# Performance work log

Hardware: AMD Instinct MI355X
Metric: run time of the kernel (lower is better)

## Reference

```python
import jax, jax.numpy as jnp
import numpy as np

NUM_SKILLS = 50000
HIDDEN = 64
B, T = 8192, 1024
EPS = 1e-6


def setup_inputs() -> dict:
    key = jax.random.key(0)
    ks = jax.random.split(key, 8)
    X = jax.random.randint(ks[0], (B,), 0, NUM_SKILLS)
    y = jax.random.randint(ks[1], (B, T), 0, 2, dtype=jnp.int32)
    embed = jax.random.normal(ks[2], (NUM_SKILLS, HIDDEN), jnp.float32)
    bound = 1.0 / np.sqrt(HIDDEN)
    W0 = jax.random.uniform(ks[3], (HIDDEN, HIDDEN), jnp.float32, -bound, bound)
    b0 = jnp.zeros((HIDDEN,), jnp.float32)
    W1 = jax.random.uniform(ks[4], (HIDDEN, HIDDEN), jnp.float32, -bound, bound)
    b1 = jnp.zeros((HIDDEN,), jnp.float32)
    Wout = jax.random.uniform(ks[5], (HIDDEN, 4), jnp.float32, -bound, bound)
    bout = jnp.zeros((4,), jnp.float32)
    return {"X": X, "y": y, "embed": embed, "W0": W0, "b0": b0,
            "W1": W1, "b1": b1, "Wout": Wout, "bout": bout}


def reference(X, y, embed, W0, b0, W1, b1, Wout, bout):
    # Per-student BKT params from embedding + 2-layer MLP + sigmoid, clamped
    h = embed[X]                                   # (B, H)
    h = jax.nn.relu(h @ W0 + b0)
    h = jax.nn.relu(h @ W1 + b1)
    params = jnp.clip(jax.nn.sigmoid(h @ Wout + bout), EPS, 1.0 - EPS)  # (B, 4)
    l, g, s, prior = params[:, 0], params[:, 1], params[:, 2], params[:, 3]

    def step(latent, y_t):
        true_correct = jnp.where(y_t == -1, 0, y_t)
        correct = latent * (1.0 - s) + (1.0 - latent) * g
        k_t1 = latent * (1.0 - s) / correct
        k_t0 = latent * s / (latent * s + (1.0 - latent) * (1.0 - g))
        k_t = jnp.where(true_correct > 0.5, k_t1, k_t0)
        next_latent = jnp.clip(k_t + (1.0 - k_t) * l, EPS, 1.0 - EPS)
        return next_latent, (correct, latent)

    _, (corrects, latents) = jax.lax.scan(step, prior, y.T)  # scan over T
    return corrects.T, latents.T                            # (B, T) each
```

## Files before the change

kernel.cpp:

```cpp
#include <hip/hip_runtime.h>

#define HIDDEN 64
#define TSTEPS 1024
#define NROWS  8192
#define NCHUNK 16
#define CLEN   64
#define KEPS   1e-6f

__global__ __launch_bounds__(64) void bkt_mlp_kernel(
    const int* __restrict__ X, const float* __restrict__ embed,
    const float* __restrict__ W0, const float* __restrict__ b0,
    const float* __restrict__ W1, const float* __restrict__ b1,
    const float* __restrict__ Wout, const float* __restrict__ bout,
    float4* __restrict__ params)
{
    const int row = blockIdx.x;
    const int j   = threadIdx.x;
    __shared__ float sh[HIDDEN];

    const int skill = X[row];
    sh[j] = embed[skill * HIDDEN + j];
    __syncthreads();

    float acc = b0[j];
    #pragma unroll
    for (int k = 0; k < HIDDEN; ++k)
        acc = fmaf(sh[k], W0[k * HIDDEN + j], acc);
    float h0 = fmaxf(acc, 0.0f);
    __syncthreads();
    sh[j] = h0;
    __syncthreads();

    acc = b1[j];
    #pragma unroll
    for (int k = 0; k < HIDDEN; ++k)
        acc = fmaf(sh[k], W1[k * HIDDEN + j], acc);
    float h1 = fmaxf(acc, 0.0f);

    float p0 = h1 * Wout[j * 4 + 0];
    float p1 = h1 * Wout[j * 4 + 1];
    float p2 = h1 * Wout[j * 4 + 2];
    float p3 = h1 * Wout[j * 4 + 3];
    #pragma unroll
    for (int off = 32; off >= 1; off >>= 1) {
        p0 += __shfl_down(p0, off, 64);
        p1 += __shfl_down(p1, off, 64);
        p2 += __shfl_down(p2, off, 64);
        p3 += __shfl_down(p3, off, 64);
    }
    if (j == 0) {
        float v0 = p0 + bout[0], v1 = p1 + bout[1], v2 = p2 + bout[2], v3 = p3 + bout[3];
        float4 r;
        r.x = fminf(fmaxf(1.0f / (1.0f + __expf(-v0)), KEPS), 1.0f - KEPS);
        r.y = fminf(fmaxf(1.0f / (1.0f + __expf(-v1)), KEPS), 1.0f - KEPS);
        r.z = fminf(fmaxf(1.0f / (1.0f + __expf(-v2)), KEPS), 1.0f - KEPS);
        r.w = fminf(fmaxf(1.0f / (1.0f + __expf(-v3)), KEPS), 1.0f - KEPS);
        params[row] = r;
    }
}

__global__ __launch_bounds__(64) void bkt_chunk_mats(
    const int* __restrict__ y, const float4* __restrict__ params,
    float4* __restrict__ Mbuf, unsigned long long* __restrict__ maskbuf)
{
    const int lane = threadIdx.x;
    const int base = blockIdx.x * 64;
    const int c    = blockIdx.y;
    const int t0   = c * CLEN;

    unsigned long long mask = 0ull;
    #pragma unroll 8
    for (int r = 0; r < 64; ++r) {
        int val = y[(size_t)(base + r) * TSTEPS + t0 + lane];
        unsigned long long bal = __ballot(val > 0);
        if (lane == r) mask = bal;
    }

    const float4 p = params[base + lane];
    const float l = p.x, g = p.y, s = p.z;
    const float c1 = 1.f - s - g, d1 = g;
    const float e00_1 = fmaf(l, c1, (1.f - l) * (1.f - s));
    const float e01_1 = l * d1;
    const float c0 = s + g - 1.f, d0 = 1.f - g;
    const float e00_0 = fmaf(l, c0, (1.f - l) * s);
    const float e01_0 = l * d0;

    float m00 = 1.f, m01 = 0.f, m10 = 0.f, m11 = 1.f;
    #pragma unroll
    for (int tt = 0; tt < CLEN; ++tt) {
        const bool one = (mask >> tt) & 1ull;
        const float e00 = one ? e00_1 : e00_0;
        const float e01 = one ? e01_1 : e01_0;
        const float e10 = one ? c1 : c0;
        const float e11 = one ? d1 : d0;
        float n00 = fmaf(e00, m00, e01 * m10);
        float n01 = fmaf(e00, m01, e01 * m11);
        float n10 = fmaf(e10, m00, e11 * m10);
        float n11 = fmaf(e10, m01, e11 * m11);
        if ((tt & 3) == 3) {
            float inv = __builtin_amdgcn_rcpf(n11);
            m00 = n00 * inv; m01 = n01 * inv; m10 = n10 * inv; m11 = 1.f;
        } else {
            m00 = n00; m01 = n01; m10 = n10; m11 = n11;
        }
    }
    Mbuf  [(size_t)c * NROWS + base + lane] = make_float4(m00, m01, m10, m11);
    maskbuf[(size_t)c * NROWS + base + lane] = mask;
}

__global__ __launch_bounds__(256) void bkt_chunk_starts(
    const float4* __restrict__ params, const float4* __restrict__ Mbuf,
    float* __restrict__ L0buf)
{
    const int r = blockIdx.x * 256 + threadIdx.x;
    float L = params[r].w;
    #pragma unroll
    for (int c = 0; c < NCHUNK; ++c) {
        L0buf[(size_t)c * NROWS + r] = L;
        float4 M = Mbuf[(size_t)c * NROWS + r];
        float num = fmaf(M.x, L, M.y);
        float den = fmaf(M.z, L, M.w);
        L = num * __builtin_amdgcn_rcpf(den);
        L = fminf(fmaxf(L, KEPS), 1.f - KEPS);
    }
}

__global__ __launch_bounds__(64) void bkt_chunk_scan(
    const float4* __restrict__ params, const unsigned long long* __restrict__ maskbuf,
    const float* __restrict__ L0buf,
    float* __restrict__ out_corr, float* __restrict__ out_lat)
{
    const int lane = threadIdx.x;
    const int base = blockIdx.x * 64;
    const int c    = blockIdx.y;
    const int row  = base + lane;

    __shared__ float scor[64][17];
    __shared__ float slat[64][17];

    const float4 p = params[row];
    const float l = p.x, g = p.y, s = p.z;
    const float a   = 1.f - s;
    const float c1v = a - g;
    const float omg = 1.f - g;
    const float c2v = s - omg;
    const float oml = 1.f - l;

    const unsigned long long mask = maskbuf[(size_t)c * NROWS + row];
    float L = L0buf[(size_t)c * NROWS + row];

    const int subr = lane >> 4;
    const int tq   = lane & 15;

    for (int gq = 0; gq < 4; ++gq) {
        #pragma unroll
        for (int q = 0; q < 16; ++q) {
            const int tt = gq * 16 + q;
            const float correct = fmaf(L, c1v, g);
            const float den0    = fmaf(L, c2v, omg);
            const float k1 = (L * a) * __builtin_amdgcn_rcpf(correct);
            const float k0 = (L * s) * __builtin_amdgcn_rcpf(den0);
            const bool one = (mask >> tt) & 1ull;
            const float k = one ? k1 : k0;
            scor[lane][q] = correct;
            slat[lane][q] = L;
            L = fminf(fmaxf(fmaf(k, oml, l), KEPS), 1.f - KEPS);
        }
        __syncthreads();
        #pragma unroll
        for (int it = 0; it < 16; ++it) {
            const int rr = it * 4 + subr;
            const size_t o = (size_t)(base + rr) * TSTEPS + c * CLEN + gq * 16 + tq;
            out_corr[o] = scor[rr][tq];
            out_lat [o] = slat[rr][tq];
        }
        __syncthreads();
    }
}

extern "C" void kernel_launch(void* const* d_in, const int* in_sizes, int n_in,
                              void* d_out, int out_size, void* d_ws, size_t ws_size,
                              hipStream_t stream) {
    const int*   X     = (const int*)  d_in[0];
    const int*   y     = (const int*)  d_in[1];
    const float* embed = (const float*)d_in[2];
    const float* W0    = (const float*)d_in[3];
    const float* b0    = (const float*)d_in[4];
    const float* W1    = (const float*)d_in[5];
    const float* b1    = (const float*)d_in[6];
    const float* Wout  = (const float*)d_in[7];
    const float* bout  = (const float*)d_in[8];

    float* out_corr = (float*)d_out;
    float* out_lat  = out_corr + (size_t)NROWS * TSTEPS;

    char* ws = (char*)d_ws;
    float4*             paramsb = (float4*)(ws);
    float4*             Mbuf    = (float4*)(ws + (128 << 10));
    unsigned long long* maskbuf = (unsigned long long*)(ws + (128 << 10) + (2 << 20));
    float*              L0buf   = (float*)(ws + (128 << 10) + (3 << 20));

    bkt_mlp_kernel<<<NROWS, 64, 0, stream>>>(X, embed, W0, b0, W1, b1, Wout, bout, paramsb);
    bkt_chunk_mats<<<dim3(NROWS / 64, NCHUNK), 64, 0, stream>>>(y, paramsb, Mbuf, maskbuf);
    bkt_chunk_starts<<<NROWS / 256, 256, 0, stream>>>(paramsb, Mbuf, L0buf);
    bkt_chunk_scan<<<dim3(NROWS / 64, NCHUNK), 64, 0, stream>>>(paramsb, maskbuf, L0buf, out_corr, out_lat);
}
```

Baseline: 141.7 us.

## Fuse MLP, chunk matrices, chunk-start scan and output scan into one kernel

```diff
diff --git a/kernel.cpp b/kernel.cpp
--- a/kernel.cpp
+++ b/kernel.cpp
@@ -1,83 +1,113 @@
 #include <hip/hip_runtime.h>
 
-#define HIDDEN 64
 #define TSTEPS 1024
 #define NROWS  8192
 #define NCHUNK 16
 #define CLEN   64
 #define KEPS   1e-6f
 
-__global__ __launch_bounds__(64) void bkt_mlp_kernel(
-    const int* __restrict__ X, const float* __restrict__ embed,
+__global__ __launch_bounds__(64) void bkt_fused(
+    const int* __restrict__ X, const int* __restrict__ y,
+    const float* __restrict__ embed,
     const float* __restrict__ W0, const float* __restrict__ b0,
     const float* __restrict__ W1, const float* __restrict__ b1,
     const float* __restrict__ Wout, const float* __restrict__ bout,
-    float4* __restrict__ params)
+    float* __restrict__ out_corr, float* __restrict__ out_lat)
 {
-    const int row = blockIdx.x;
-    const int j   = threadIdx.x;
-    __shared__ float sh[HIDDEN];
-
-    const int skill = X[row];
-    sh[j] = embed[skill * HIDDEN + j];
+    const int lane    = threadIdx.x;
+    const int rowbase = blockIdx.x * 4;
+
+    __shared__ float sh[4][64];
+
+    #pragma unroll
+    for (int rs = 0; rs < 4; ++rs) {
+        const int skill = X[rowbase + rs];
+        sh[rs][lane] = embed[(size_t)skill * 64 + lane];
+    }
     __syncthreads();
 
-    float acc = b0[j];
-    #pragma unroll
-    for (int k = 0; k < HIDDEN; ++k)
-        acc = fmaf(sh[k], W0[k * HIDDEN + j], acc);
-    float h0 = fmaxf(acc, 0.0f);
+    float a0 = b0[lane], a1 = a0, a2 = a0, a3 = a0;
+    #pragma unroll
+    for (int k4 = 0; k4 < 16; ++k4) {
+        const float4 e0 = *(const float4*)&sh[0][k4 * 4];
+        const float4 e1 = *(const float4*)&sh[1][k4 * 4];
+        const float4 e2 = *(const float4*)&sh[2][k4 * 4];
+        const float4 e3 = *(const float4*)&sh[3][k4 * 4];
+        const float w0 = W0[(k4 * 4 + 0) * 64 + lane];
+        const float w1 = W0[(k4 * 4 + 1) * 64 + lane];
+        const float w2 = W0[(k4 * 4 + 2) * 64 + lane];
+        const float w3 = W0[(k4 * 4 + 3) * 64 + lane];
+        a0 = fmaf(e0.x, w0, a0); a0 = fmaf(e0.y, w1, a0); a0 = fmaf(e0.z, w2, a0); a0 = fmaf(e0.w, w3, a0);
+        a1 = fmaf(e1.x, w0, a1); a1 = fmaf(e1.y, w1, a1); a1 = fmaf(e1.z, w2, a1); a1 = fmaf(e1.w, w3, a1);
+        a2 = fmaf(e2.x, w0, a2); a2 = fmaf(e2.y, w1, a2); a2 = fmaf(e2.z, w2, a2); a2 = fmaf(e2.w, w3, a2);
+        a3 = fmaf(e3.x, w0, a3); a3 = fmaf(e3.y, w1, a3); a3 = fmaf(e3.z, w2, a3); a3 = fmaf(e3.w, w3, a3);
+    }
     __syncthreads();
-    sh[j] = h0;
+    sh[0][lane] = fmaxf(a0, 0.f);
+    sh[1][lane] = fmaxf(a1, 0.f);
+    sh[2][lane] = fmaxf(a2, 0.f);
+    sh[3][lane] = fmaxf(a3, 0.f);
     __syncthreads();
 
-    acc = b1[j];
-    #pragma unroll
-    for (int k = 0; k < HIDDEN; ++k)
-        acc = fmaf(sh[k], W1[k * HIDDEN + j], acc);
-    float h1 = fmaxf(acc, 0.0f);
-
-    float p0 = h1 * Wout[j * 4 + 0];
-    float p1 = h1 * Wout[j * 4 + 1];
-    float p2 = h1 * Wout[j * 4 + 2];
-    float p3 = h1 * Wout[j * 4 + 3];
+    a0 = b1[lane]; a1 = a0; a2 = a0; a3 = a0;
+    #pragma unroll
+    for (int k4 = 0; k4 < 16; ++k4) {
+        const float4 e0 = *(const float4*)&sh[0][k4 * 4];
+        const float4 e1 = *(const float4*)&sh[1][k4 * 4];
+        const float4 e2 = *(const float4*)&sh[2][k4 * 4];
+        const float4 e3 = *(const float4*)&sh[3][k4 * 4];
+        const float w0 = W1[(k4 * 4 + 0) * 64 + lane];
+        const float w1 = W1[(k4 * 4 + 1) * 64 + lane];
+        const float w2 = W1[(k4 * 4 + 2) * 64 + lane];
+        const float w3 = W1[(k4 * 4 + 3) * 64 + lane];
+        a0 = fmaf(e0.x, w0, a0); a0 = fmaf(e0.y, w1, a0); a0 = fmaf(e0.z, w2, a0); a0 = fmaf(e0.w, w3, a0);
+        a1 = fmaf(e1.x, w0, a1); a1 = fmaf(e1.y, w1, a1); a1 = fmaf(e1.z, w2, a1); a1 = fmaf(e1.w, w3, a1);
+        a2 = fmaf(e2.x, w0, a2); a2 = fmaf(e2.y, w1, a2); a2 = fmaf(e2.z, w2, a2); a2 = fmaf(e2.w, w3, a2);
+        a3 = fmaf(e3.x, w0, a3); a3 = fmaf(e3.y, w1, a3); a3 = fmaf(e3.z, w2, a3); a3 = fmaf(e3.w, w3, a3);
+    }
+    const float h0r = fmaxf(a0, 0.f), h1r = fmaxf(a1, 0.f);
+    const float h2r = fmaxf(a2, 0.f), h3r = fmaxf(a3, 0.f);
+
+    const float4 wo = ((const float4*)Wout)[lane];
+    float p[4][4];
+    p[0][0] = h0r * wo.x; p[0][1] = h0r * wo.y; p[0][2] = h0r * wo.z; p[0][3] = h0r * wo.w;
+    p[1][0] = h1r * wo.x; p[1][1] = h1r * wo.y; p[1][2] = h1r * wo.z; p[1][3] = h1r * wo.w;
+    p[2][0] = h2r * wo.x; p[2][1] = h2r * wo.y; p[2][2] = h2r * wo.z; p[2][3] = h2r * wo.w;
+    p[3][0] = h3r * wo.x; p[3][1] = h3r * wo.y; p[3][2] = h3r * wo.z; p[3][3] = h3r * wo.w;
     #pragma unroll
     for (int off = 32; off >= 1; off >>= 1) {
-        p0 += __shfl_down(p0, off, 64);
-        p1 += __shfl_down(p1, off, 64);
-        p2 += __shfl_down(p2, off, 64);
-        p3 += __shfl_down(p3, off, 64);
-    }
-    if (j == 0) {
-        float v0 = p0 + bout[0], v1 = p1 + bout[1], v2 = p2 + bout[2], v3 = p3 + bout[3];
-        float4 r;
-        r.x = fminf(fmaxf(1.0f / (1.0f + __expf(-v0)), KEPS), 1.0f - KEPS);
-        r.y = fminf(fmaxf(1.0f / (1.0f + __expf(-v1)), KEPS), 1.0f - KEPS);
-        r.z = fminf(fmaxf(1.0f / (1.0f + __expf(-v2)), KEPS), 1.0f - KEPS);
-        r.w = fminf(fmaxf(1.0f / (1.0f + __expf(-v3)), KEPS), 1.0f - KEPS);
-        params[row] = r;
-    }
-}
-
-__global__ __launch_bounds__(64) void bkt_chunk_mats(
-    const int* __restrict__ y, const float4* __restrict__ params,
-    float4* __restrict__ Mbuf, unsigned long long* __restrict__ maskbuf)
-{
-    const int lane = threadIdx.x;
-    const int base = blockIdx.x * 64;
-    const int c    = blockIdx.y;
-    const int t0   = c * CLEN;
+        #pragma unroll
+        for (int rs = 0; rs < 4; ++rs)
+            #pragma unroll
+            for (int c = 0; c < 4; ++c)
+                p[rs][c] += __shfl_xor(p[rs][c], off, 64);
+    }
+    const float4 bo = *(const float4*)bout;
+
+    const int rsme = lane >> 4;
+    const int cme  = lane & 15;
+    float v0 = (rsme == 0) ? p[0][0] : (rsme == 1) ? p[1][0] : (rsme == 2) ? p[2][0] : p[3][0];
+    float v1 = (rsme == 0) ? p[0][1] : (rsme == 1) ? p[1][1] : (rsme == 2) ? p[2][1] : p[3][1];
+    float v2 = (rsme == 0) ? p[0][2] : (rsme == 1) ? p[1][2] : (rsme == 2) ? p[2][2] : p[3][2];
+    float v3 = (rsme == 0) ? p[0][3] : (rsme == 1) ? p[1][3] : (rsme == 2) ? p[2][3] : p[3][3];
+    v0 += bo.x; v1 += bo.y; v2 += bo.z; v3 += bo.w;
+
+    const float l     = fminf(fmaxf(1.0f / (1.0f + __expf(-v0)), KEPS), 1.0f - KEPS);
+    const float g     = fminf(fmaxf(1.0f / (1.0f + __expf(-v1)), KEPS), 1.0f - KEPS);
+    const float s     = fminf(fmaxf(1.0f / (1.0f + __expf(-v2)), KEPS), 1.0f - KEPS);
+    const float prior = fminf(fmaxf(1.0f / (1.0f + __expf(-v3)), KEPS), 1.0f - KEPS);
 
     unsigned long long mask = 0ull;
-    #pragma unroll 8
-    for (int r = 0; r < 64; ++r) {
-        int val = y[(size_t)(base + r) * TSTEPS + t0 + lane];
-        unsigned long long bal = __ballot(val > 0);
-        if (lane == r) mask = bal;
-    }
-
-    const float4 p = params[base + lane];
-    const float l = p.x, g = p.y, s = p.z;
+    #pragma unroll
+    for (int rs = 0; rs < 4; ++rs) {
+        #pragma unroll
+        for (int c = 0; c < 16; ++c) {
+            const int val = y[(size_t)(rowbase + rs) * TSTEPS + c * CLEN + lane];
+            const unsigned long long bal = __ballot(val > 0);
+            if (lane == rs * 16 + c) mask = bal;
+        }
+    }
+
     const float c1 = 1.f - s - g, d1 = g;
     const float e00_1 = fmaf(l, c1, (1.f - l) * (1.f - s));
     const float e01_1 = l * d1;
@@ -98,83 +128,58 @@
         float n10 = fmaf(e10, m00, e11 * m10);
         float n11 = fmaf(e10, m01, e11 * m11);
         if ((tt & 3) == 3) {
-            float inv = __builtin_amdgcn_rcpf(n11);
+            const float inv = __builtin_amdgcn_rcpf(n11);
             m00 = n00 * inv; m01 = n01 * inv; m10 = n10 * inv; m11 = 1.f;
         } else {
             m00 = n00; m01 = n01; m10 = n10; m11 = n11;
         }
     }
-    Mbuf  [(size_t)c * NROWS + base + lane] = make_float4(m00, m01, m10, m11);
-    maskbuf[(size_t)c * NROWS + base + lane] = mask;
-}
-
-__global__ __launch_bounds__(256) void bkt_chunk_starts(
-    const float4* __restrict__ params, const float4* __restrict__ Mbuf,
-    float* __restrict__ L0buf)
-{
-    const int r = blockIdx.x * 256 + threadIdx.x;
-    float L = params[r].w;
-    #pragma unroll
-    for (int c = 0; c < NCHUNK; ++c) {
-        L0buf[(size_t)c * NROWS + r] = L;
-        float4 M = Mbuf[(size_t)c * NROWS + r];
-        float num = fmaf(M.x, L, M.y);
-        float den = fmaf(M.z, L, M.w);
+
+    const int grp = lane & 48;
+    float L  = prior;
+    float L0 = prior;
+    #pragma unroll
+    for (int cc = 0; cc < 16; ++cc) {
+        const float q00 = __shfl(m00, grp | cc, 64);
+        const float q01 = __shfl(m01, grp | cc, 64);
+        const float q10 = __shfl(m10, grp | cc, 64);
+        const float q11 = __shfl(m11, grp | cc, 64);
+        if (cme == cc) L0 = L;
+        const float num = fmaf(q00, L, q01);
+        const float den = fmaf(q10, L, q11);
         L = num * __builtin_amdgcn_rcpf(den);
         L = fminf(fmaxf(L, KEPS), 1.f - KEPS);
     }
-}
-
-__global__ __launch_bounds__(64) void bkt_chunk_scan(
-    const float4* __restrict__ params, const unsigned long long* __restrict__ maskbuf,
-    const float* __restrict__ L0buf,
-    float* __restrict__ out_corr, float* __restrict__ out_lat)
-{
-    const int lane = threadIdx.x;
-    const int base = blockIdx.x * 64;
-    const int c    = blockIdx.y;
-    const int row  = base + lane;
-
-    __shared__ float scor[64][17];
-    __shared__ float slat[64][17];
-
-    const float4 p = params[row];
-    const float l = p.x, g = p.y, s = p.z;
-    const float a   = 1.f - s;
-    const float c1v = a - g;
-    const float omg = 1.f - g;
-    const float c2v = s - omg;
-    const float oml = 1.f - l;
-
-    const unsigned long long mask = maskbuf[(size_t)c * NROWS + row];
-    float L = L0buf[(size_t)c * NROWS + row];
-
-    const int subr = lane >> 4;
-    const int tq   = lane & 15;
-
-    for (int gq = 0; gq < 4; ++gq) {
+
+    const float a    = 1.f - s;
+    const float c1v  = a - g;
+    const float omg  = 1.f - g;
+    const float c2v  = s - omg;
+    const float oml  = 1.f - l;
+
+    const size_t obase = (size_t)(rowbase + rsme) * TSTEPS + cme * CLEN;
+    float Lc = L0;
+    #pragma unroll
+    for (int w = 0; w < 4; ++w) {
+        float cr[4], lt[4];
         #pragma unroll
         for (int q = 0; q < 16; ++q) {
-            const int tt = gq * 16 + q;
-            const float correct = fmaf(L, c1v, g);
-            const float den0    = fmaf(L, c2v, omg);
-            const float k1 = (L * a) * __builtin_amdgcn_rcpf(correct);
-            const float k0 = (L * s) * __builtin_amdgcn_rcpf(den0);
+            const int tt = w * 16 + q;
+            const float correct = fmaf(Lc, c1v, g);
+            const float den0    = fmaf(Lc, c2v, omg);
+            const float k1 = (Lc * a) * __builtin_amdgcn_rcpf(correct);
+            const float k0 = (Lc * s) * __builtin_amdgcn_rcpf(den0);
             const bool one = (mask >> tt) & 1ull;
             const float k = one ? k1 : k0;
-            scor[lane][q] = correct;
-            slat[lane][q] = L;
-            L = fminf(fmaxf(fmaf(k, oml, l), KEPS), 1.f - KEPS);
+            cr[q & 3] = correct;
+            lt[q & 3] = Lc;
+            Lc = fminf(fmaxf(fmaf(k, oml, l), KEPS), 1.f - KEPS);
+            if ((q & 3) == 3) {
+                const size_t o = obase + w * 16 + (q - 3);
+                *(float4*)&out_corr[o] = make_float4(cr[0], cr[1], cr[2], cr[3]);
+                *(float4*)&out_lat [o] = make_float4(lt[0], lt[1], lt[2], lt[3]);
+            }
         }
-        __syncthreads();
-        #pragma unroll
-        for (int it = 0; it < 16; ++it) {
-            const int rr = it * 4 + subr;
-            const size_t o = (size_t)(base + rr) * TSTEPS + c * CLEN + gq * 16 + tq;
-            out_corr[o] = scor[rr][tq];
-            out_lat [o] = slat[rr][tq];
-        }
-        __syncthreads();
     }
 }
 
@@ -194,14 +199,6 @@
     float* out_corr = (float*)d_out;
     float* out_lat  = out_corr + (size_t)NROWS * TSTEPS;
 
-    char* ws = (char*)d_ws;
-    float4*             paramsb = (float4*)(ws);
-    float4*             Mbuf    = (float4*)(ws + (128 << 10));
-    unsigned long long* maskbuf = (unsigned long long*)(ws + (128 << 10) + (2 << 20));
-    float*              L0buf   = (float*)(ws + (128 << 10) + (3 << 20));
-
-    bkt_mlp_kernel<<<NROWS, 64, 0, stream>>>(X, embed, W0, b0, W1, b1, Wout, bout, paramsb);
-    bkt_chunk_mats<<<dim3(NROWS / 64, NCHUNK), 64, 0, stream>>>(y, paramsb, Mbuf, maskbuf);
-    bkt_chunk_starts<<<NROWS / 256, 256, 0, stream>>>(paramsb, Mbuf, L0buf);
-    bkt_chunk_scan<<<dim3(NROWS / 64, NCHUNK), 64, 0, stream>>>(paramsb, maskbuf, L0buf, out_corr, out_lat);
+    bkt_fused<<<NROWS / 4, 64, 0, stream>>>(X, y, embed, W0, b0, W1, b1, Wout, bout,
+                                            out_corr, out_lat);
 }
```

New measurement: 136.3 us. -3.8%, faster.
